# Kernel tuning notes

Measured on AMD Instinct MI355X. Metric: run time of the kernel, lower is better.

## Reference

```python
import jax, jax.numpy as jnp
import numpy as np

T, B, D, H = 110, 256, 512, 512
EPS = 1e-9


def _forward(a, v, l, qmask, umask, mu_a, mu_v, mu_l, shifta, shiftv,
             turna, turnb, W1, b1, W2, b2):
    Tcur = a.shape[0]
    # ca = mu * (cos(a) + i sin(a)) = mu * exp(i a)
    ca = mu_a[:Tcur] * jnp.exp(1j * a)          # (T,B,D) complex64
    cv = mu_v[:Tcur] * jnp.exp(1j * v)
    cl = mu_l[:Tcur] * jnp.exp(1j * l)
    # phase shift of a and v streams, then sum into lav
    features = cl + ca * jnp.exp(1j * shifta) + cv * jnp.exp(1j * shiftv)  # (T,B,D)

    # --- step 0 (special-cased in the original loop) ---
    temp0 = features[0]                          # (B,D) complex
    qa0 = qmask[0][:, 0:1]                       # (B,1)
    qb0 = qmask[0][:, 1:2]
    ones = jnp.ones_like(temp0) * (1.0 + 1.0j)   # pA=pB=1+1j initial state
    pA0 = (1.0 - qa0) * ones + qa0 * temp0
    pB0 = (1.0 - qb0) * ones + qb0 * temp0

    # --- steps 1..T-1 as a fused scan over time ---
    def step(carry, xs):
        pA, pB = carry
        f, qm, ta, tb = xs                       # f:(B,D) cplx, qm:(B,2), ta/tb:(1,D)
        qa = qm[:, 0:1]
        qb = qm[:, 1:2]
        turn = qa * (pA * jnp.exp(1j * ta)) + qb * (pB * jnp.exp(1j * tb))
        # torch: turn.where(turn==0, turn/(abs+eps)) -> keep 0 where 0, else normalize
        turn = jnp.where(turn == 0, turn, turn / (jnp.abs(turn) + EPS))
        temp = f + turn
        pA = (1.0 - qa) * pA + qa * temp
        pB = (1.0 - qb) * pB + qb * temp
        return (pA, pB), temp

    (_, _), temps = jax.lax.scan(
        step, (pA0, pB0),
        (features[1:], qmask[1:], turna[1:Tcur], turnb[1:Tcur]))

    feats = jnp.concatenate([temp0[None], temps], axis=0)  # (T,B,D) complex
    fr, fi = feats.real, feats.imag
    f1r = fr @ W1.T + b1
    f1i = fi @ W1.T + b1
    f2r = fr @ W2.T + b2
    f2i = fi @ W2.T + b2
    xr = f1r - f2i
    xi = f1i + f2r
    return xr + xi                               # (T,B,H) float32


def setup_inputs() -> dict:
    key = jax.random.key(0)
    ks = jax.random.split(key, 12)
    a = jax.random.normal(ks[0], (T, B, D), jnp.float32)
    v = jax.random.normal(ks[1], (T, B, D), jnp.float32)
    l = jax.random.normal(ks[2], (T, B, D), jnp.float32)
    spk = jax.random.randint(ks[3], (T, B), 0, 2)
    qmask = jax.nn.one_hot(spk, 2, dtype=jnp.float32)      # (T,B,2)
    umask = jnp.ones((T, B), jnp.float32)                  # unused by forward
    mu_a = jnp.ones((110, 1, 1), jnp.float32)
    mu_v = jnp.ones((110, 1, 1), jnp.float32)
    mu_l = jnp.ones((110, 1, 1), jnp.float32)
    shifta = jax.random.normal(ks[4], (1, 1, D), jnp.float32)
    shiftv = jax.random.normal(ks[5], (1, 1, D), jnp.float32)
    turna = jax.random.uniform(ks[6], (110, 1, D), jnp.float32)
    turnb = jax.random.uniform(ks[7], (110, 1, D), jnp.float32)
    W1 = jax.random.normal(ks[8], (H, D), jnp.float32) * 0.02
    b1 = jnp.zeros((H,), jnp.float32)
    W2 = jax.random.normal(ks[9], (H, D), jnp.float32) * 0.02
    b2 = jnp.zeros((H,), jnp.float32)
    return {"a": a, "v": v, "l": l, "qmask": qmask, "umask": umask,
            "mu_a": mu_a, "mu_v": mu_v, "mu_l": mu_l,
            "shifta": shifta, "shiftv": shiftv,
            "turna": turna, "turnb": turnb,
            "W1": W1, "b1": b1, "W2": W2, "b2": b2,
            "dia_len": T}


def reference(a, v, l, qmask, umask, mu_a, mu_v, mu_l, shifta, shiftv,
              turna, turnb, W1, b1, W2, b2, dia_len):
    return _forward(a, v, l, qmask, umask, mu_a, mu_v, mu_l,
                    shifta, shiftv, turna, turnb, W1, b1, W2, b2)
```

## Files before the change

### kernel.cpp

```cpp
#include <hip/hip_runtime.h>

#define T_DIM 110
#define B_DIM 256
#define D_DIM 512
#define H_DIM 512
#define K_CAT 1024
#define M_DIM (T_DIM * B_DIM)
#define BD    (B_DIM * D_DIM)
#define EPSV 1e-9f

typedef float f32x4 __attribute__((ext_vector_type(4)));
typedef short bf16x8 __attribute__((ext_vector_type(8)));

static __device__ __forceinline__ unsigned short f2bf(float f) {
    unsigned u = __builtin_bit_cast(unsigned, f);
    u += 0x7fffu + ((u >> 16) & 1u);
    return (unsigned short)(u >> 16);
}

__global__ __launch_bounds__(256) void prep_w_kernel(
    const float* __restrict__ W1, const float* __restrict__ b1,
    const float* __restrict__ W2,
    unsigned short* __restrict__ Bt,
    float* __restrict__ bias2)
{
    int i = blockIdx.x * 256 + threadIdx.x;
    if (i < H_DIM) bias2[i] = 2.0f * b1[i];
    if (i >= H_DIM * K_CAT) return;
    int h = i / K_CAT;
    int k = i % K_CAT;
    int j = k >> 1;
    float w = (k & 1) ? (W1[h * D_DIM + j] - W2[h * D_DIM + j])
                      : (W1[h * D_DIM + j] + W2[h * D_DIM + j]);
    Bt[i] = f2bf(w);
}

__global__ __launch_bounds__(256) void prep_tt_kernel(
    const float* __restrict__ turna, const float* __restrict__ turnb,
    float4* __restrict__ TT)
{
    int i = blockIdx.x * 256 + threadIdx.x;
    if (i >= T_DIM * D_DIM) return;
    float s1, c1, s2, c2;
    __sincosf(turna[i], &s1, &c1);
    __sincosf(turnb[i], &s2, &c2);
    TT[i] = make_float4(c1, s1, c2, s2);
}

__global__ __launch_bounds__(256) void feat_scan_kernel(
    const float* __restrict__ a, const float* __restrict__ v,
    const float* __restrict__ l, const float* __restrict__ qmask,
    const float* __restrict__ mu_a, const float* __restrict__ mu_v,
    const float* __restrict__ mu_l,
    const float* __restrict__ shifta, const float* __restrict__ shiftv,
    const float4* __restrict__ TT,
    unsigned int* __restrict__ A32)
{
    __shared__ float qm_s[T_DIM], mua_s[T_DIM], muv_s[T_DIM], mul_s[T_DIM];
    const int tx = threadIdx.x;
    const int b  = blockIdx.x >> 1;
    const int d  = ((blockIdx.x & 1) << 8) + tx;
    if (tx < T_DIM) {
        qm_s[tx]  = qmask[(size_t)(tx * B_DIM + b) * 2];
        mua_s[tx] = mu_a[tx];
        muv_s[tx] = mu_v[tx];
        mul_s[tx] = mu_l[tx];
    }
    const float sa = shifta[d];
    const float sv = shiftv[d];
    __syncthreads();

    const size_t gbase = (size_t)b * D_DIM + d;

#define LDSET(A_,V_,L_,T4_,Q_,MA_,MV_,ML_, tt_)                                \
    { const int t_ = (tt_);                                                    \
      A_  = a[(size_t)t_ * BD + gbase];                                        \
      V_  = v[(size_t)t_ * BD + gbase];                                        \
      L_  = l[(size_t)t_ * BD + gbase];                                        \
      T4_ = TT[t_ * D_DIM + d];                                                \
      Q_  = qm_s[t_]; MA_ = mua_s[t_]; MV_ = muv_s[t_]; ML_ = mul_s[t_]; }

    float a0,v0,l0,q0,ma0,mv0,ml0; float4 tt0;
    float a1,v1,l1,q1,ma1,mv1,ml1; float4 tt1;
    float a2,v2,l2,q2,ma2,mv2,ml2; float4 tt2;
    LDSET(a0,v0,l0,tt0,q0,ma0,mv0,ml0, 0)
    LDSET(a1,v1,l1,tt1,q1,ma1,mv1,ml1, 1)
    LDSET(a2,v2,l2,tt2,q2,ma2,mv2,ml2, 2)

    float pAr = 1.f, pAi = 1.f, pBr = 1.f, pBi = 1.f;

    #pragma unroll 3
    for (int t = 0; t < T_DIM; ++t) {
        float aN,vN,lN,qN,maN,mvN,mlN; float4 ttN;
        const int tp = (t + 3 < T_DIM) ? t + 3 : T_DIM - 1;
        LDSET(aN,vN,lN,ttN,qN,maN,mvN,mlN, tp)
        __builtin_amdgcn_sched_barrier(0);

        float sA,cA,sV,cV,sL,cL;
        __sincosf(a0 + sa, &sA, &cA);
        __sincosf(v0 + sv, &sV, &cV);
        __sincosf(l0,      &sL, &cL);
        float fr = ml0 * cL + ma0 * cA + mv0 * cV;
        float fi = ml0 * sL + ma0 * sA + mv0 * sV;

        const bool isA = q0 > 0.5f;
        const float cp = isA ? tt0.x : tt0.z;
        const float sp = isA ? tt0.y : tt0.w;
        const float pr = isA ? pAr : pBr;
        const float pi = isA ? pAi : pBi;
        float tr = pr * cp - pi * sp;
        float ti = pr * sp + pi * cp;
        const float gate = (t == 0) ? 0.0f : 1.0f;
        const float inv = gate / (sqrtf(tr * tr + ti * ti) + EPSV);
        fr += tr * inv;
        fi += ti * inv;
        pAr = isA ? fr : pAr;  pAi = isA ? fi : pAi;
        pBr = isA ? pBr : fr;  pBi = isA ? pBi : fi;

        A32[(size_t)(t * B_DIM + b) * (K_CAT / 2) + d] =
            (unsigned)f2bf(fr) | ((unsigned)f2bf(fi) << 16);

        a0=a1; v0=v1; l0=l1; tt0=tt1; q0=q1; ma0=ma1; mv0=mv1; ml0=ml1;
        a1=a2; v1=v2; l1=l2; tt1=tt2; q1=q2; ma1=ma2; mv1=mv2; ml1=ml2;
        a2=aN; v2=vN; l2=lN; tt2=ttN; q2=qN; ma2=maN; mv2=mvN; ml2=mlN;
    }
#undef LDSET
}

#define BM 128
#define BN 128
#define BK 64

__global__ __launch_bounds__(256) void gemm_kernel(
    const unsigned short* __restrict__ A,
    const unsigned short* __restrict__ Bt,
    const float* __restrict__ bias2,
    float* __restrict__ C)
{
    __shared__ __align__(16) unsigned short As[BM * BK];
    __shared__ __align__(16) unsigned short Bs[BN * BK];

    const int tid = threadIdx.x;
    const int wave = tid >> 6;
    const int lane = tid & 63;
    const int wr = wave >> 1;
    const int wc = wave & 1;
    const int m0 = blockIdx.x * BM;
    const int n0 = blockIdx.y * BN;
    const int lrow = lane & 15;
    const int lk8 = (lane >> 4) * 8;

    const int srow = wave * 32;
    const int lrow8 = lane >> 3;
    const int lchunk = lane & 7;

    f32x4 acc[4][4] = {};

    for (int k0 = 0; k0 < K_CAT; k0 += BK) {
        #pragma unroll
        for (int c = 0; c < 4; ++c) {
            const int row = srow + c * 8 + lrow8;
            {
                const unsigned short* gp = A + (size_t)(m0 + row) * K_CAT + k0 + lchunk * 8;
                unsigned short* lp = As + (srow + c * 8) * BK + lane * 8;
                __builtin_amdgcn_global_load_lds(
                    (const __attribute__((address_space(1))) unsigned int*)gp,
                    (__attribute__((address_space(3))) unsigned int*)lp,
                    16, 0, 0);
            }
            {
                const unsigned short* gp = Bt + (size_t)(n0 + row) * K_CAT + k0 + lchunk * 8;
                unsigned short* lp = Bs + (srow + c * 8) * BK + lane * 8;
                __builtin_amdgcn_global_load_lds(
                    (const __attribute__((address_space(1))) unsigned int*)gp,
                    (__attribute__((address_space(3))) unsigned int*)lp,
                    16, 0, 0);
            }
        }
        __syncthreads();

        bf16x8 af[4][2], bfv[4][2];
        #pragma unroll
        for (int m = 0; m < 4; ++m)
            #pragma unroll
            for (int kk = 0; kk < 2; ++kk)
                af[m][kk] = *reinterpret_cast<const bf16x8*>(
                    &As[(wr * 64 + m * 16 + lrow) * BK + kk * 32 + lk8]);
        #pragma unroll
        for (int n = 0; n < 4; ++n)
            #pragma unroll
            for (int kk = 0; kk < 2; ++kk)
                bfv[n][kk] = *reinterpret_cast<const bf16x8*>(
                    &Bs[(wc * 64 + n * 16 + lrow) * BK + kk * 32 + lk8]);

        #pragma unroll
        for (int kk = 0; kk < 2; ++kk)
            #pragma unroll
            for (int m = 0; m < 4; ++m)
                #pragma unroll
                for (int n = 0; n < 4; ++n)
                    acc[m][n] = __builtin_amdgcn_mfma_f32_16x16x32_bf16(
                        af[m][kk], bfv[n][kk], acc[m][n], 0, 0, 0);
        __syncthreads();
    }

    const int rbase = m0 + wr * 64 + (lane >> 4) * 4;
    const int cbase = n0 + wc * 64;
    #pragma unroll
    for (int n = 0; n < 4; ++n) {
        const int col = cbase + n * 16 + lrow;
        const float bv = bias2[col];
        #pragma unroll
        for (int m = 0; m < 4; ++m) {
            const int row0 = rbase + m * 16;
            #pragma unroll
            for (int r = 0; r < 4; ++r) {
                C[(size_t)(row0 + r) * H_DIM + col] = acc[m][n][r] + bv;
            }
        }
    }
}

extern "C" void kernel_launch(void* const* d_in, const int* in_sizes, int n_in,
                              void* d_out, int out_size, void* d_ws, size_t ws_size,
                              hipStream_t stream) {
    const float* a      = (const float*)d_in[0];
    const float* v      = (const float*)d_in[1];
    const float* l      = (const float*)d_in[2];
    const float* qmask  = (const float*)d_in[3];
    const float* mu_a   = (const float*)d_in[5];
    const float* mu_v   = (const float*)d_in[6];
    const float* mu_l   = (const float*)d_in[7];
    const float* shifta = (const float*)d_in[8];
    const float* shiftv = (const float*)d_in[9];
    const float* turna  = (const float*)d_in[10];
    const float* turnb  = (const float*)d_in[11];
    const float* W1     = (const float*)d_in[12];
    const float* b1     = (const float*)d_in[13];
    const float* W2     = (const float*)d_in[14];
    float* out = (float*)d_out;

    char* ws = (char*)d_ws;
    unsigned short* Afeat = (unsigned short*)ws;
    size_t offB  = (size_t)M_DIM * K_CAT * sizeof(unsigned short);
    unsigned short* Bt = (unsigned short*)(ws + offB);
    size_t offBias = offB + (size_t)H_DIM * K_CAT * sizeof(unsigned short);
    float* bias2 = (float*)(ws + offBias);
    size_t offTT = offBias + 4096;
    float4* TT = (float4*)(ws + offTT);

    prep_w_kernel<<<(H_DIM * K_CAT + 255) / 256, 256, 0, stream>>>(W1, b1, W2, Bt, bias2);
    prep_tt_kernel<<<(T_DIM * D_DIM + 255) / 256, 256, 0, stream>>>(turna, turnb, TT);
    feat_scan_kernel<<<B_DIM * 2, 256, 0, stream>>>(
        a, v, l, qmask, mu_a, mu_v, mu_l, shifta, shiftv, TT, (unsigned int*)Afeat);
    dim3 grid(M_DIM / BM, H_DIM / BN);
    gemm_kernel<<<grid, 256, 0, stream>>>(Afeat, Bt, bias2, out);
}
```

Measured before the change: 113.5 us.

## Double-buffer GEMM LDS tiles and deepen scan prefetch with rsq normalization

The GEMM now double-buffers its A and B LDS tiles so the next K-tile's global-to-LDS loads are issued while MFMAs run on the current tile, which is meant to hide load latency behind compute. The scan kernel is manually unrolled by four, keeping a four-deep register prefetch ring instead of shifting three-deep copies each step. It also replaces the sqrt-plus-divide normalization with a hardware reciprocal square root clamped by fmaxf. The extra LDS buffer halves the number of GEMM blocks that fit per CU. The rsq path also changes precision and the eps behavior slightly.

Result: slower. 127.0 us (+11.9%).

```diff
diff --git a/kernel.cpp b/kernel.cpp
--- a/kernel.cpp
+++ b/kernel.cpp
@@ -72,64 +72,73 @@
 
     const size_t gbase = (size_t)b * D_DIM + d;
 
-#define LDSET(A_,V_,L_,T4_,Q_,MA_,MV_,ML_, tt_)                                \
-    { const int t_ = (tt_);                                                    \
-      A_  = a[(size_t)t_ * BD + gbase];                                        \
-      V_  = v[(size_t)t_ * BD + gbase];                                        \
-      L_  = l[(size_t)t_ * BD + gbase];                                        \
-      T4_ = TT[t_ * D_DIM + d];                                                \
-      Q_  = qm_s[t_]; MA_ = mua_s[t_]; MV_ = muv_s[t_]; ML_ = mul_s[t_]; }
-
-    float a0,v0,l0,q0,ma0,mv0,ml0; float4 tt0;
-    float a1,v1,l1,q1,ma1,mv1,ml1; float4 tt1;
-    float a2,v2,l2,q2,ma2,mv2,ml2; float4 tt2;
-    LDSET(a0,v0,l0,tt0,q0,ma0,mv0,ml0, 0)
-    LDSET(a1,v1,l1,tt1,q1,ma1,mv1,ml1, 1)
-    LDSET(a2,v2,l2,tt2,q2,ma2,mv2,ml2, 2)
+    float  s0a = a[gbase],                 s0v = v[gbase],
+           s0l = l[gbase];
+    float4 s0t = TT[d];
+    float  s1a = a[(size_t)1 * BD + gbase], s1v = v[(size_t)1 * BD + gbase],
+           s1l = l[(size_t)1 * BD + gbase];
+    float4 s1t = TT[1 * D_DIM + d];
+    float  s2a = a[(size_t)2 * BD + gbase], s2v = v[(size_t)2 * BD + gbase],
+           s2l = l[(size_t)2 * BD + gbase];
+    float4 s2t = TT[2 * D_DIM + d];
+    float  s3a = a[(size_t)3 * BD + gbase], s3v = v[(size_t)3 * BD + gbase],
+           s3l = l[(size_t)3 * BD + gbase];
+    float4 s3t = TT[3 * D_DIM + d];
 
     float pAr = 1.f, pAi = 1.f, pBr = 1.f, pBi = 1.f;
 
-    #pragma unroll 3
-    for (int t = 0; t < T_DIM; ++t) {
-        float aN,vN,lN,qN,maN,mvN,mlN; float4 ttN;
-        const int tp = (t + 3 < T_DIM) ? t + 3 : T_DIM - 1;
-        LDSET(aN,vN,lN,ttN,qN,maN,mvN,mlN, tp)
-        __builtin_amdgcn_sched_barrier(0);
-
-        float sA,cA,sV,cV,sL,cL;
-        __sincosf(a0 + sa, &sA, &cA);
-        __sincosf(v0 + sv, &sV, &cV);
-        __sincosf(l0,      &sL, &cL);
-        float fr = ml0 * cL + ma0 * cA + mv0 * cV;
-        float fi = ml0 * sL + ma0 * sA + mv0 * sV;
-
-        const bool isA = q0 > 0.5f;
-        const float cp = isA ? tt0.x : tt0.z;
-        const float sp = isA ? tt0.y : tt0.w;
-        const float pr = isA ? pAr : pBr;
-        const float pi = isA ? pAi : pBi;
-        float tr = pr * cp - pi * sp;
-        float ti = pr * sp + pi * cp;
-        const float gate = (t == 0) ? 0.0f : 1.0f;
-        const float inv = gate / (sqrtf(tr * tr + ti * ti) + EPSV);
-        fr += tr * inv;
-        fi += ti * inv;
-        pAr = isA ? fr : pAr;  pAi = isA ? fi : pAi;
-        pBr = isA ? pBr : fr;  pBi = isA ? pBi : fi;
-
-        A32[(size_t)(t * B_DIM + b) * (K_CAT / 2) + d] =
-            (unsigned)f2bf(fr) | ((unsigned)f2bf(fi) << 16);
-
-        a0=a1; v0=v1; l0=l1; tt0=tt1; q0=q1; ma0=ma1; mv0=mv1; ml0=ml1;
-        a1=a2; v1=v2; l1=l2; tt1=tt2; q1=q2; ma1=ma2; mv1=mv2; ml1=ml2;
-        a2=aN; v2=vN; l2=lN; tt2=ttN; q2=qN; ma2=maN; mv2=mvN; ml2=mlN;
-    }
-#undef LDSET
+#define ITER(tt_, SA_, SV_, SL_, ST_)                                          \
+    {                                                                          \
+        const int t_ = (tt_);                                                  \
+        const float qa = qm_s[t_], ma = mua_s[t_],                             \
+                    mv = muv_s[t_], ml = mul_s[t_];                            \
+        float sA, cA, sV, cV, sL, cL;                                          \
+        __sincosf(SA_ + sa, &sA, &cA);                                         \
+        __sincosf(SV_ + sv, &sV, &cV);                                         \
+        __sincosf(SL_,      &sL, &cL);                                         \
+        float fr = ml * cL + ma * cA + mv * cV;                                \
+        float fi = ml * sL + ma * sA + mv * sV;                                \
+        const bool isA = qa > 0.5f;                                            \
+        const float cp = isA ? ST_.x : ST_.z;                                  \
+        const float sp = isA ? ST_.y : ST_.w;                                  \
+        const float pr = isA ? pAr : pBr;                                      \
+        const float pi = isA ? pAi : pBi;                                      \
+        const float tr = pr * cp - pi * sp;                                    \
+        const float ti = pr * sp + pi * cp;                                    \
+        const float gate = (t_ == 0) ? 0.0f : 1.0f;                            \
+        const float m2 = fmaxf(tr * tr + ti * ti, 1e-30f);                     \
+        const float inv = gate * __builtin_amdgcn_rsqf(m2);                    \
+        fr += tr * inv;                                                        \
+        fi += ti * inv;                                                        \
+        pAr = isA ? fr : pAr;  pAi = isA ? fi : pAi;                           \
+        pBr = isA ? pBr : fr;  pBi = isA ? pBi : fi;                           \
+        A32[(size_t)(t_ * B_DIM + b) * (K_CAT / 2) + d] =                      \
+            (unsigned)f2bf(fr) | ((unsigned)f2bf(fi) << 16);                   \
+                   \
+        const int tnx = (t_ + 4 < T_DIM) ? t_ + 4 : T_DIM - 1;                 \
+        SA_ = a[(size_t)tnx * BD + gbase];                                     \
+        SV_ = v[(size_t)tnx * BD + gbase];                                     \
+        SL_ = l[(size_t)tnx * BD + gbase];                                     \
+        ST_ = TT[(size_t)tnx * D_DIM + d];                                     \
+                  \
+        __builtin_amdgcn_sched_barrier(0x387);                                 \
+    }
+
+    for (int tb = 0; tb < 108; tb += 4) {
+        ITER(tb,     s0a, s0v, s0l, s0t)
+        ITER(tb + 1, s1a, s1v, s1l, s1t)
+        ITER(tb + 2, s2a, s2v, s2l, s2t)
+        ITER(tb + 3, s3a, s3v, s3l, s3t)
+    }
+    ITER(108, s0a, s0v, s0l, s0t)
+    ITER(109, s1a, s1v, s1l, s1t)
+#undef ITER
 }
 
 #define BM 128
 #define BN 128
 #define BK 64
+#define NT (K_CAT / BK)
 
 __global__ __launch_bounds__(256) void gemm_kernel(
     const unsigned short* __restrict__ A,
@@ -137,8 +146,8 @@
     const float* __restrict__ bias2,
     float* __restrict__ C)
 {
-    __shared__ __align__(16) unsigned short As[BM * BK];
-    __shared__ __align__(16) unsigned short Bs[BN * BK];
+    __shared__ __align__(16) unsigned short As[2][BM * BK];
+    __shared__ __align__(16) unsigned short Bs[2][BN * BK];
 
     const int tid = threadIdx.x;
     const int wave = tid >> 6;
@@ -154,30 +163,37 @@
     const int lrow8 = lane >> 3;
     const int lchunk = lane & 7;
 
+#define STAGE(buf_, k0_)                                                       \
+    {                                                                          \
+        const int kk0 = (k0_);                                                 \
+        _Pragma("unroll")                                                      \
+        for (int c = 0; c < 4; ++c) {                                          \
+            const int row = srow + c * 8 + lrow8;                              \
+            const unsigned short* gpA =                                        \
+                A + (size_t)(m0 + row) * K_CAT + kk0 + lchunk * 8;             \
+            unsigned short* lpA = &As[buf_][(srow + c * 8) * BK + lane * 8];   \
+            __builtin_amdgcn_global_load_lds(                                  \
+                (const __attribute__((address_space(1))) unsigned int*)gpA,    \
+                (__attribute__((address_space(3))) unsigned int*)lpA,          \
+                16, 0, 0);                                                     \
+            const unsigned short* gpB =                                        \
+                Bt + (size_t)(n0 + row) * K_CAT + kk0 + lchunk * 8;            \
+            unsigned short* lpB = &Bs[buf_][(srow + c * 8) * BK + lane * 8];   \
+            __builtin_amdgcn_global_load_lds(                                  \
+                (const __attribute__((address_space(1))) unsigned int*)gpB,    \
+                (__attribute__((address_space(3))) unsigned int*)lpB,          \
+                16, 0, 0);                                                     \
+        }                                                                      \
+    }
+
     f32x4 acc[4][4] = {};
 
-    for (int k0 = 0; k0 < K_CAT; k0 += BK) {
-        #pragma unroll
-        for (int c = 0; c < 4; ++c) {
-            const int row = srow + c * 8 + lrow8;
-            {
-                const unsigned short* gp = A + (size_t)(m0 + row) * K_CAT + k0 + lchunk * 8;
-                unsigned short* lp = As + (srow + c * 8) * BK + lane * 8;
-                __builtin_amdgcn_global_load_lds(
-                    (const __attribute__((address_space(1))) unsigned int*)gp,
-                    (__attribute__((address_space(3))) unsigned int*)lp,
-                    16, 0, 0);
-            }
-            {
-                const unsigned short* gp = Bt + (size_t)(n0 + row) * K_CAT + k0 + lchunk * 8;
-                unsigned short* lp = Bs + (srow + c * 8) * BK + lane * 8;
-                __builtin_amdgcn_global_load_lds(
-                    (const __attribute__((address_space(1))) unsigned int*)gp,
-                    (__attribute__((address_space(3))) unsigned int*)lp,
-                    16, 0, 0);
-            }
-        }
-        __syncthreads();
+    STAGE(0, 0);
+    __syncthreads();
+
+    for (int t = 0; t < NT; ++t) {
+        const int cur = t & 1;
+        if (t + 1 < NT) STAGE(cur ^ 1, (t + 1) * BK);
 
         bf16x8 af[4][2], bfv[4][2];
         #pragma unroll
@@ -185,13 +201,13 @@
             #pragma unroll
             for (int kk = 0; kk < 2; ++kk)
                 af[m][kk] = *reinterpret_cast<const bf16x8*>(
-                    &As[(wr * 64 + m * 16 + lrow) * BK + kk * 32 + lk8]);
+                    &As[cur][(wr * 64 + m * 16 + lrow) * BK + kk * 32 + lk8]);
         #pragma unroll
         for (int n = 0; n < 4; ++n)
             #pragma unroll
             for (int kk = 0; kk < 2; ++kk)
                 bfv[n][kk] = *reinterpret_cast<const bf16x8*>(
-                    &Bs[(wc * 64 + n * 16 + lrow) * BK + kk * 32 + lk8]);
+                    &Bs[cur][(wc * 64 + n * 16 + lrow) * BK + kk * 32 + lk8]);
 
         #pragma unroll
         for (int kk = 0; kk < 2; ++kk)
@@ -201,8 +217,10 @@
                 for (int n = 0; n < 4; ++n)
                     acc[m][n] = __builtin_amdgcn_mfma_f32_16x16x32_bf16(
                         af[m][kk], bfv[n][kk], acc[m][n], 0, 0, 0);
+
         __syncthreads();
     }
+#undef STAGE
 
     const int rbase = m0 + wr * 64 + (lane >> 4) * 4;
     const int cbase = n0 + wc * 64;
```
